# Kernel tuning notes

Measured on AMD Instinct MI355X. Metric: run time of the kernel, lower is better.

The kernel has to match this reference:

```python
import jax, jax.numpy as jnp
import numpy as np

# ---- static config (matches init_kwargs) ----
B, N_CAMS, C, H, W = 2, 6, 256, 32, 88
BEV_H = BEV_W = 100
NQ = BEV_H * BEV_W
D_PILLAR = 4
HEADS = 8
LEVELS = 3
HEAD_DIM = C // HEADS
PC_RANGE = (-51.2, -51.2, -5.0, 51.2, 51.2, 3.0)
OGFH, OGFW = 256, 704


def _make_lidar2img():
    """Plausible lidar->image projection matrices (K @ [R|t]) for 6 ring cameras."""
    mats = np.zeros((B, N_CAMS, 4, 4), np.float32)
    K = np.array([[557.0, 0.0, OGFW / 2.0], [0.0, 557.0, OGFH / 2.0], [0.0, 0.0, 1.0]], np.float64)
    for b in range(B):
        for n in range(N_CAMS):
            yaw = 2.0 * np.pi * n / N_CAMS + 0.05 * b
            fwd = np.array([np.cos(yaw), np.sin(yaw), 0.0])
            right = np.array([np.sin(yaw), -np.cos(yaw), 0.0])
            down = np.array([0.0, 0.0, -1.0])
            R = np.stack([right, down, fwd])  # lidar -> camera axes
            cam_center = np.array([1.5 * np.cos(yaw), 1.5 * np.sin(yaw), 1.8])
            t = -R @ cam_center
            P = K @ np.concatenate([R, t[:, None]], axis=1)
            mats[b, n, :3, :] = P.astype(np.float32)
            mats[b, n, 3, 3] = 1.0
    return jnp.asarray(mats)


def setup_inputs() -> dict:
    key = jax.random.key(0)
    ks = jax.random.split(key, 16)
    s = 0.02
    return {
        'imgs': jax.random.normal(ks[0], (B, N_CAMS, C, H, W), jnp.float32),
        'lidar2img': _make_lidar2img(),
        'bev_query': jax.random.normal(ks[1], (NQ, 1, C), jnp.float32) * s,
        'bev_pos': jax.random.normal(ks[2], (1, NQ, C), jnp.float32) * s,
        'cams_embeds': jax.random.normal(ks[3], (N_CAMS, C), jnp.float32) * s,
        'level_embeds': jax.random.normal(ks[4], (LEVELS, C), jnp.float32) * s,
        'w_fpn': jax.random.normal(ks[5], (LEVELS, C, C), jnp.float32) * s,
        'b_fpn': jnp.zeros((LEVELS, C), jnp.float32),
        'w_value': jax.random.normal(ks[6], (C, C), jnp.float32) * s,
        'b_value': jnp.zeros((C,), jnp.float32),
        'w_off': jax.random.normal(ks[7], (C, HEADS * LEVELS * D_PILLAR * 2), jnp.float32) * s,
        'b_off': jax.random.normal(ks[8], (HEADS * LEVELS * D_PILLAR * 2,), jnp.float32) * 0.5,
        'w_attn': jax.random.normal(ks[9], (C, HEADS * LEVELS * D_PILLAR), jnp.float32) * s,
        'b_attn': jnp.zeros((HEADS * LEVELS * D_PILLAR,), jnp.float32),
        'w_out': jax.random.normal(ks[10], (C, C), jnp.float32) * s,
        'b_out': jnp.zeros((C,), jnp.float32),
        'w_ts1': jax.random.normal(ks[11], (C, C), jnp.float32) * s,
        'b_ts1': jnp.zeros((C,), jnp.float32),
        'w_ts2': jax.random.normal(ks[12], (C, C), jnp.float32) * s,
        'b_ts2': jnp.zeros((C,), jnp.float32),
    }


def _deform_sample(v, loc, h, w):
    """Bilinear sample (grid_sample, zero padding, align_corners=False).
    v: [N, heads, h*w, dh]; loc: [N, heads, Q, 2] normalized to [0,1]. -> [N, heads, Q, dh]"""
    x = loc[..., 0] * w - 0.5
    y = loc[..., 1] * h - 0.5
    x0 = jnp.floor(x)
    y0 = jnp.floor(y)
    out = jnp.zeros(v.shape[:2] + (loc.shape[2], v.shape[-1]), v.dtype)
    for dx in (0, 1):
        for dy in (0, 1):
            xi = x0 + dx
            yi = y0 + dy
            wgt = (1.0 - jnp.abs(x - xi)) * (1.0 - jnp.abs(y - yi))
            valid = (xi >= 0) & (xi < w) & (yi >= 0) & (yi < h)
            idx = (jnp.clip(yi, 0, h - 1) * w + jnp.clip(xi, 0, w - 1)).astype(jnp.int32)
            g = jnp.take_along_axis(v, idx[..., None], axis=2)
            out = out + g * (wgt * valid)[..., None]
    return out


def _forward(imgs, lidar2img, bev_query, bev_pos, cams_embeds, level_embeds,
             w_fpn, b_fpn, w_value, b_value, w_off, b_off, w_attn, b_attn,
             w_out, b_out, w_ts1, b_ts1, w_ts2, b_ts2):
    # ---- FPN: 3 levels at strides 1/2/4 with per-level 1x1 projection ----
    x = imgs.reshape(B * N_CAMS, C, H, W)
    feats, shapes = [], []
    cur = x
    for l in range(LEVELS):
        if l > 0:
            bn, c, h, w = cur.shape
            cur = cur.reshape(bn, c, h // 2, 2, w // 2, 2).mean(axis=(3, 5))
        f = jnp.einsum('bchw,cd->bdhw', cur, w_fpn[l]) + b_fpn[l][None, :, None, None]
        feats.append(f)
        shapes.append((f.shape[2], f.shape[3]))
    # ---- flatten levels + cam/level embeds: [N, sum_hw, B, C] ----
    flat = []
    for l, f in enumerate(feats):
        h, w = shapes[l]
        fl = jnp.transpose(f.reshape(B, N_CAMS, C, h * w), (1, 0, 3, 2))  # [N,B,hw,C]
        fl = fl + cams_embeds[:, None, None, :] + level_embeds[l][None, None, None, :]
        flat.append(fl)
    feat_flatten = jnp.transpose(jnp.concatenate(flat, axis=2), (0, 2, 1, 3))  # [N,sum_hw,B,C]

    # ---- 3D pillar reference points, normalized [0,1] ----
    zrange = PC_RANGE[5] - PC_RANGE[2]
    zs = jnp.linspace(0.5, zrange - 0.5, D_PILLAR) / zrange
    xs = (jnp.arange(BEV_W, dtype=jnp.float32) + 0.5) / BEV_W
    ys = (jnp.arange(BEV_H, dtype=jnp.float32) + 0.5) / BEV_H
    gy, gx = jnp.meshgrid(ys, xs, indexing='ij')
    ref2d = jnp.stack([gx.ravel(), gy.ravel()], axis=-1)  # [NQ,2]
    ref3d = jnp.concatenate([
        jnp.broadcast_to(ref2d[None], (D_PILLAR, NQ, 2)),
        jnp.broadcast_to(zs[:, None, None].astype(jnp.float32), (D_PILLAR, NQ, 1)),
    ], axis=-1)
    scale = jnp.array([PC_RANGE[3] - PC_RANGE[0], PC_RANGE[4] - PC_RANGE[1], zrange], jnp.float32)
    shift = jnp.array(PC_RANGE[:3], jnp.float32)
    xyz = ref3d * scale + shift
    homog = jnp.concatenate([xyz, jnp.ones((D_PILLAR, NQ, 1), jnp.float32)], axis=-1)

    # ---- point sampling: project to each camera, mask invalid pixels ----
    pts = jnp.einsum('bnij,dqj->nbqdi', lidar2img, homog)  # [N,B,NQ,D,4]
    eps = 1e-5
    depth = pts[..., 2]
    xy = pts[..., :2] / jnp.maximum(depth[..., None], eps)
    ref_cam = xy / jnp.array([OGFW, OGFH], jnp.float32)  # [N,B,NQ,D,2]
    bev_mask = ((depth > eps) & (ref_cam[..., 0] > 0) & (ref_cam[..., 0] < 1)
                & (ref_cam[..., 1] > 0) & (ref_cam[..., 1] < 1))  # [N,B,NQ,D]

    pos = bev_pos[0]  # [NQ,C]

    def sca(query, value, ref_b, mask_b):
        # query [NQ,C]; value [N,sum_hw,C]; ref_b [N,NQ,D,2]; mask_b [N,NQ,D]
        residual = query
        q = query + pos
        v = value @ w_value + b_value
        off = (q @ w_off + b_off).reshape(NQ, HEADS, LEVELS, D_PILLAR, 2)
        attn = jax.nn.softmax((q @ w_attn + b_attn).reshape(NQ, HEADS, LEVELS * D_PILLAR), axis=-1)
        attn = attn.reshape(NQ, HEADS, LEVELS, D_PILLAR)
        out = jnp.zeros((N_CAMS, NQ, HEADS, HEAD_DIM), q.dtype)
        start = 0
        for l, (h, w) in enumerate(shapes):
            hw = h * w
            v_l = jnp.transpose(v[:, start:start + hw].reshape(N_CAMS, hw, HEADS, HEAD_DIM), (0, 2, 1, 3))
            start += hw
            norm = jnp.array([w, h], q.dtype)
            loc = ref_b[:, :, None, :, :] + off[None, :, :, l] / norm  # [N,NQ,heads,D,2]
            loc = jnp.transpose(loc, (0, 2, 1, 3, 4)).reshape(N_CAMS, HEADS, NQ * D_PILLAR, 2)
            s = _deform_sample(v_l, loc, h, w).reshape(N_CAMS, HEADS, NQ, D_PILLAR, HEAD_DIM)
            out = out + jnp.einsum('nhqpd,qhp->nqhd', s, attn[:, :, l])
        out = out.reshape(N_CAMS, NQ, C)
        valid = mask_b.any(axis=-1)  # [N,NQ]
        slots = (out * valid[..., None].astype(out.dtype)).sum(axis=0)
        count = jnp.maximum(valid.sum(axis=0), 1).astype(out.dtype)[:, None]
        slots = slots / count
        return slots @ w_out + b_out + residual

    def tsblock(t):
        return jax.nn.relu(t @ w_ts1 + b_ts1) @ w_ts2 + b_ts2

    bq = jnp.transpose(bev_query, (1, 0, 2))[0]  # [NQ,C]
    groups = []
    ego = bq
    for b in range(B):
        val = feat_flatten[:, :, b, :]
        r = ref_cam[:, b]
        m = bev_mask[:, b]
        if b == 0:
            for _ in range(2):
                bq = tsblock(sca(bq, val, r, m))
            ego = bq
            groups.append(ego.reshape(C, BEV_W, BEV_H))
        else:
            nb = tsblock(sca(ego, val, r, m))
            groups.append(nb.reshape(C, BEV_W, BEV_H))
    bev_groups = jnp.stack(groups, axis=0)  # [B,C,BEV_W,BEV_H]
    return bq[None], bev_groups


def reference(imgs, lidar2img, bev_query, bev_pos, cams_embeds, level_embeds,
              w_fpn, b_fpn, w_value, b_value, w_off, b_off, w_attn, b_attn,
              w_out, b_out, w_ts1, b_ts1, w_ts2, b_ts2):
    return _forward(imgs, lidar2img, bev_query, bev_pos, cams_embeds, level_embeds,
                    w_fpn, b_fpn, w_value, b_value, w_off, b_off, w_attn, b_attn,
                    w_out, b_out, w_ts1, b_ts1, w_ts2, b_ts2)
```

## Files before the change

### kernel.cpp

```cpp
#include <hip/hip_runtime.h>
#include <math.h>

typedef __attribute__((ext_vector_type(8))) short bf16x8;
typedef __attribute__((ext_vector_type(4))) float f32x4;

__device__ __forceinline__ unsigned short f2bf(float x) {
  union { float f; unsigned int u; } v; v.f = x;
  unsigned int r = v.u + 0x7fffu + ((v.u >> 16) & 1u);
  return (unsigned short)(r >> 16);
}
__device__ __forceinline__ float bf2f(unsigned short b) {
  union { unsigned int u; float f; } v; v.u = ((unsigned int)b) << 16; return v.f;
}
__device__ __forceinline__ void split2(float x, unsigned short& h, unsigned short& l) {
  h = f2bf(x);
  l = f2bf(x - bf2f(h));
}
__device__ __forceinline__ int fsi(int q, int c) { return q * 256 + (c ^ ((q & 7) << 2)); }

__device__ __forceinline__ void writeP(unsigned short* __restrict__ P, int col, int k,
                                       unsigned short h, unsigned short l) {
  int tile = col >> 4;
  int lane = (((k >> 3) & 3) << 4) | (col & 15);
  int ks = k >> 5, j8 = k & 7;
  size_t base = ((size_t)(tile >> 1) * 16384) + (size_t)(((tile & 1) << 4) + ks * 2) * 512
              + (size_t)lane * 8 + j8;
  P[base] = h;
  P[base + 512] = l;
}

__device__ __forceinline__ void ld16(const unsigned short* b, bf16x8* f) {
  const unsigned short* b1 = b + 2048;
  const unsigned short* b2 = b + 4096;
  const unsigned short* b3 = b + 6144;
  asm volatile(
    "global_load_dwordx4 %0, %16, off\n\t"
    "global_load_dwordx4 %1, %16, off offset:1024\n\t"
    "global_load_dwordx4 %2, %16, off offset:2048\n\t"
    "global_load_dwordx4 %3, %16, off offset:3072\n\t"
    "global_load_dwordx4 %4, %17, off\n\t"
    "global_load_dwordx4 %5, %17, off offset:1024\n\t"
    "global_load_dwordx4 %6, %17, off offset:2048\n\t"
    "global_load_dwordx4 %7, %17, off offset:3072\n\t"
    "global_load_dwordx4 %8, %18, off\n\t"
    "global_load_dwordx4 %9, %18, off offset:1024\n\t"
    "global_load_dwordx4 %10, %18, off offset:2048\n\t"
    "global_load_dwordx4 %11, %18, off offset:3072\n\t"
    "global_load_dwordx4 %12, %19, off\n\t"
    "global_load_dwordx4 %13, %19, off offset:1024\n\t"
    "global_load_dwordx4 %14, %19, off offset:2048\n\t"
    "global_load_dwordx4 %15, %19, off offset:3072\n\t"
    "s_waitcnt vmcnt(0)"
    : "=&v"(f[0]), "=&v"(f[1]), "=&v"(f[2]), "=&v"(f[3]),
      "=&v"(f[4]), "=&v"(f[5]), "=&v"(f[6]), "=&v"(f[7]),
      "=&v"(f[8]), "=&v"(f[9]), "=&v"(f[10]), "=&v"(f[11]),
      "=&v"(f[12]), "=&v"(f[13]), "=&v"(f[14]), "=&v"(f[15])
    : "v"(b), "v"(b1), "v"(b2), "v"(b3));
}

__device__ __forceinline__ void ld16nw(const unsigned short* b, bf16x8* f) {
  const unsigned short* b1 = b + 2048;
  const unsigned short* b2 = b + 4096;
  const unsigned short* b3 = b + 6144;
  asm volatile(
    "global_load_dwordx4 %0, %16, off\n\t"
    "global_load_dwordx4 %1, %16, off offset:1024\n\t"
    "global_load_dwordx4 %2, %16, off offset:2048\n\t"
    "global_load_dwordx4 %3, %16, off offset:3072\n\t"
    "global_load_dwordx4 %4, %17, off\n\t"
    "global_load_dwordx4 %5, %17, off offset:1024\n\t"
    "global_load_dwordx4 %6, %17, off offset:2048\n\t"
    "global_load_dwordx4 %7, %17, off offset:3072\n\t"
    "global_load_dwordx4 %8, %18, off\n\t"
    "global_load_dwordx4 %9, %18, off offset:1024\n\t"
    "global_load_dwordx4 %10, %18, off offset:2048\n\t"
    "global_load_dwordx4 %11, %18, off offset:3072\n\t"
    "global_load_dwordx4 %12, %19, off\n\t"
    "global_load_dwordx4 %13, %19, off offset:1024\n\t"
    "global_load_dwordx4 %14, %19, off offset:2048\n\t"
    "global_load_dwordx4 %15, %19, off offset:3072"
    : "=&v"(f[0]), "=&v"(f[1]), "=&v"(f[2]), "=&v"(f[3]),
      "=&v"(f[4]), "=&v"(f[5]), "=&v"(f[6]), "=&v"(f[7]),
      "=&v"(f[8]), "=&v"(f[9]), "=&v"(f[10]), "=&v"(f[11]),
      "=&v"(f[12]), "=&v"(f[13]), "=&v"(f[14]), "=&v"(f[15])
    : "v"(b), "v"(b1), "v"(b2), "v"(b3));
}

#define MFMA(a, b, c) __builtin_amdgcn_mfma_f32_16x16x32_bf16(a, b, c, 0, 0, 0)

__device__ __forceinline__ void gemm2t32(
    const unsigned short* __restrict__ Wp, int tile0,
    int lane, int lk, int l15,
    const unsigned short (&AS)[2][32][32][8], f32x4 (&acc)[2][2])
{
  const unsigned short* base = Wp + ((size_t)(tile0 >> 1) * 16384) + (size_t)lane * 8;
  bf16x8 f[32];
  ld16nw(base, f);
  ld16(base + 8192, f + 16);
  __builtin_amdgcn_sched_barrier(0);
#pragma unroll
  for (int ks = 0; ks < 8; ++ks) {
    bf16x8 h0 = f[2 * ks], l0 = f[2 * ks + 1];
    bf16x8 h1 = f[16 + 2 * ks], l1 = f[17 + 2 * ks];
#pragma unroll
    for (int nf = 0; nf < 2; ++nf) {
      bf16x8 bqh = *(const bf16x8*)&AS[0][ks * 4 + lk][nf * 16 + l15][0];
      bf16x8 bql = *(const bf16x8*)&AS[1][ks * 4 + lk][nf * 16 + l15][0];
      acc[0][nf] = MFMA(h0, bqh, acc[0][nf]);
      acc[0][nf] = MFMA(h0, bql, acc[0][nf]);
      acc[0][nf] = MFMA(l0, bqh, acc[0][nf]);
      acc[1][nf] = MFMA(h1, bqh, acc[1][nf]);
      acc[1][nf] = MFMA(h1, bql, acc[1][nf]);
      acc[1][nf] = MFMA(l1, bqh, acc[1][nf]);
    }
  }
}

__device__ __forceinline__ void gemm2t64(
    const unsigned short* __restrict__ Wp, int tile0,
    int lane, int lk, int l15,
    const unsigned short (&AS)[2][32][64][8], f32x4 (&acc)[2][4])
{
  const unsigned short* base = Wp + ((size_t)(tile0 >> 1) * 16384) + (size_t)lane * 8;
  bf16x8 f[32];
  ld16nw(base, f);
  ld16(base + 8192, f + 16);
  __builtin_amdgcn_sched_barrier(0);
#pragma unroll
  for (int ks = 0; ks < 8; ++ks) {
    bf16x8 h0 = f[2 * ks], l0 = f[2 * ks + 1];
    bf16x8 h1 = f[16 + 2 * ks], l1 = f[17 + 2 * ks];
#pragma unroll
    for (int nf = 0; nf < 4; ++nf) {
      bf16x8 bqh = *(const bf16x8*)&AS[0][ks * 4 + lk][nf * 16 + l15][0];
      bf16x8 bql = *(const bf16x8*)&AS[1][ks * 4 + lk][nf * 16 + l15][0];
      acc[0][nf] = MFMA(h0, bqh, acc[0][nf]);
      acc[0][nf] = MFMA(h0, bql, acc[0][nf]);
      acc[0][nf] = MFMA(l0, bqh, acc[0][nf]);
      acc[1][nf] = MFMA(h1, bqh, acc[1][nf]);
      acc[1][nf] = MFMA(h1, bql, acc[1][nf]);
      acc[1][nf] = MFMA(l1, bqh, acc[1][nf]);
    }
  }
}

__device__ __forceinline__ void gemm1t64(
    const unsigned short* __restrict__ Wp, int tile,
    int lane, int lk, int l15,
    const unsigned short (&AS)[2][32][64][8], f32x4 (&acc)[4])
{
  const unsigned short* base = Wp + ((size_t)(tile >> 1) * 16384) + (size_t)(tile & 1) * 8192 + (size_t)lane * 8;
  bf16x8 f[16];
  ld16(base, f);
  __builtin_amdgcn_sched_barrier(0);
#pragma unroll
  for (int ks = 0; ks < 8; ++ks) {
    bf16x8 eh = f[2 * ks], el = f[2 * ks + 1];
#pragma unroll
    for (int nf = 0; nf < 4; ++nf) {
      bf16x8 bqh = *(const bf16x8*)&AS[0][ks * 4 + lk][nf * 16 + l15][0];
      bf16x8 bql = *(const bf16x8*)&AS[1][ks * 4 + lk][nf * 16 + l15][0];
      acc[nf] = MFMA(eh, bqh, acc[nf]);
      acc[nf] = MFMA(eh, bql, acc[nf]);
      acc[nf] = MFMA(el, bqh, acc[nf]);
    }
  }
}

__global__ __launch_bounds__(256) void pool2x2(const float* __restrict__ in, float* __restrict__ out,
                                               int h, int w, int total)
{
  int i = blockIdx.x * 256 + threadIdx.x;
  if (i >= total) return;
  int x = i % w; int r = i / w; int y = r % h; int ci = r / h;
  const float* p = in + (size_t)ci * (4 * h * w) + (size_t)(2 * y) * (2 * w) + 2 * x;
  out[i] = (p[0] + p[1] + p[2 * w] + p[2 * w + 1]) * 0.25f;
}

__global__ __launch_bounds__(256) void prep(
    const float* __restrict__ wo, const float* __restrict__ bo,
    const float* __restrict__ wa, const float* __restrict__ ba,
    const float* __restrict__ wout, const float* __restrict__ wts1, const float* __restrict__ wts2,
    const float* __restrict__ wfpn, const float* __restrict__ wval,
    const float* __restrict__ cams, const float* __restrict__ lev,
    const float* __restrict__ bfpn, const float* __restrict__ bval,
    unsigned short* __restrict__ wcatP, float* __restrict__ bcat,
    unsigned short* __restrict__ woutP, unsigned short* __restrict__ wts1P,
    unsigned short* __restrict__ w45P, unsigned short* __restrict__ wcombP,
    float* __restrict__ e2)
{
  int bb = blockIdx.x, t = threadIdx.x;
  if (bb < 768) {
    int l = bb >> 8, i = bb & 255, j = t;
    const float* a = wfpn + ((size_t)l * 256 + i) * 256;
    float acc = 0.f;
    for (int k = 0; k < 256; ++k) acc = fmaf(a[k], wval[(size_t)k * 256 + j], acc);
    unsigned short h, lo; split2(acc, h, lo);
    writeP(wcombP, l * 256 + j, i, h, lo);
  } else if (bb < 1056) {
    int i = (bb - 768) * 256 + t;
    int c = i >> 8, k = i & 255;
    float v = (c < 192) ? wo[k * 192 + c] : wa[k * 96 + (c - 192)];
    unsigned short h, l; split2(v, h, l);
    writeP(wcatP, c, k, h, l);
    if (i < 288) bcat[i] = (i < 192) ? bo[i] : ba[i - 192];
  } else if (bb < 1312) {
    int i = (bb - 1056) * 256 + t;
    int nn = i >> 8, k = i & 255;
    float v = wout[(size_t)k * 256 + nn];
    unsigned short h, l; split2(v, h, l);
    writeP(woutP, nn, k, h, l);
  } else if (bb < 1568) {
    int i = (bb - 1312) * 256 + t;
    int nn = i >> 8, k = i & 255;
    float v = wts1[(size_t)k * 256 + nn];
    unsigned short h, l; split2(v, h, l);
    writeP(wts1P, nn, k, h, l);
  } else if (bb < 1824) {
    int i = (bb - 1568) * 256 + t;
    int nn = i >> 8, k = i & 255;
    float v = wts2[(size_t)k * 256 + nn];
    unsigned short h, l; split2(v, h, l);
    writeP(w45P, nn, k, h, l);
  } else if (bb < 2112) {
    int mp = bb - 1824;
    int k = t;
    float acc = 0.f;
    for (int j = 0; j < 256; ++j) {
      float wc = (mp < 192) ? wo[j * 192 + mp] : wa[j * 96 + (mp - 192)];
      acc = fmaf(wts2[(size_t)k * 256 + j], wc, acc);
    }
    unsigned short h, l; split2(acc, h, l);
    writeP(w45P, 256 + mp, k, h, l);
  } else {
    int e = bb - 2112;
    int n = e / 3, l = e % 3, j = t;
    float acc = bval[j];
    for (int k = 0; k < 256; ++k) {
      float s = cams[n * 256 + k] + lev[l * 256 + k] + bfpn[l * 256 + k];
      acc = fmaf(s, wval[(size_t)k * 256 + j], acc);
    }
    e2[(size_t)e * 256 + j] = acc;
  }
}

__global__ __launch_bounds__(512) void value_fused(
    const float* __restrict__ imgs, const float* __restrict__ cur1a, const float* __restrict__ cur2a,
    const unsigned short* __restrict__ wcombP,
    const float* __restrict__ e2, float* __restrict__ Vall)
{
  __shared__ __align__(16) unsigned short AS[2][32][32][8];
  int t = threadIdx.x, wid = t >> 6, lane = t & 63, l15 = lane & 15, lk = lane >> 4;
  int bx = blockIdx.x, cam = blockIdx.y, bz = blockIdx.z;
  const float* img0 = imgs + (size_t)bz * 4325376;
  const float* cur1 = cur1a + (size_t)bz * 1081344;
  const float* cur2 = cur2a + (size_t)bz * 270336;
  float* V = Vall + (size_t)bz * 5677056;
  int level, tb, hw; const float* src;
  if (bx < 88)       { level = 0; tb = bx;       hw = 2816; src = img0; }
  else if (bx < 110) { level = 1; tb = bx - 88;  hw = 704;  src = cur1; }
  else               { level = 2; tb = bx - 110; hw = 176;  src = cur2; }
  int p0 = tb * 32;
  const int LST[3] = {0, 2816, 3520};
  src += (size_t)cam * 256 * hw;

  {
    int pos = t & 31, kg = t >> 5;
    bool ok = (p0 + pos) < hw;
    const float* col = src + p0 + pos;
    float vals[16];
#pragma unroll
    for (int i = 0; i < 16; ++i) {
      int k = kg * 16 + i;
      vals[i] = ok ? col[(size_t)k * hw] : 0.f;
    }
#pragma unroll
    for (int half = 0; half < 2; ++half) {
      int ch = kg * 2 + half;
      bf16x8 hv, lv;
#pragma unroll
      for (int j = 0; j < 8; ++j) {
        unsigned short h, l; split2(vals[half * 8 + j], h, l);
        hv[j] = (short)h; lv[j] = (short)l;
      }
      *(bf16x8*)&AS[0][ch][pos][0] = hv;
      *(bf16x8*)&AS[1][ch][pos][0] = lv;
    }
  }
  __syncthreads();

  f32x4 zed = {0.f, 0.f, 0.f, 0.f};
  f32x4 acc[2][2] = {{zed, zed}, {zed, zed}};
  gemm2t32(wcombP, level * 16 + wid * 2, lane, lk, l15, AS, acc);
  __syncthreads();

  float* ASf = (float*)(&AS[0][0][0][0]);
  const float* bias = e2 + (size_t)(cam * 3 + level) * 256;
#pragma unroll
  for (int mf = 0; mf < 2; ++mf) {
    int chb = (wid * 2 + mf) * 16 + lk * 4;
    float4 b4 = *(const float4*)(bias + chb);
#pragma unroll
    for (int nf = 0; nf < 2; ++nf) {
      int q = nf * 16 + l15;
      float4 o;
      o.x = acc[mf][nf][0] + b4.x; o.y = acc[mf][nf][1] + b4.y;
      o.z = acc[mf][nf][2] + b4.z; o.w = acc[mf][nf][3] + b4.w;
      *(float4*)&ASf[fsi(q, chb)] = o;
    }
  }
  __syncthreads();
  float* Vb = V + ((size_t)cam * 3696 + LST[level] + p0) * 256;
#pragma unroll
  for (int j = 0; j < 4; ++j) {
    int g = t + j * 512;
    int q = g >> 6, c = (g & 63) * 4;
    if (p0 + q < hw)
      *(float4*)(Vb + (size_t)q * 256 + c) = *(const float4*)&ASf[fsi(q, c)];
  }
}

__global__ __launch_bounds__(512) void init_fused(
    const float* __restrict__ bev_pos, const float* __restrict__ bev_query,
    const float* __restrict__ bts2,
    const unsigned short* __restrict__ wcatP, const float* __restrict__ bcat,
    float* __restrict__ posA, float* __restrict__ posB,
    float* __restrict__ qtmpA, float* __restrict__ qtmpB)
{
  __shared__ __align__(16) unsigned short AS[2][32][64][8];
  float* ASf = (float*)(&AS[0][0][0][0]);
  int t = threadIdx.x, wid = t >> 6, lane = t & 63, l15 = lane & 15, lk = lane >> 4;
  int r0 = blockIdx.x * 64;
  int y = blockIdx.y;
  const float* base = y ? bev_query : bev_pos;
  const float* padd = y ? bev_pos : nullptr;
  const float* rb = y ? nullptr : bts2;
  float* oA = y ? qtmpA : posA;
  float* oB = y ? qtmpB : posB;
  f32x4 zed = {0.f, 0.f, 0.f, 0.f};

#pragma unroll
  for (int j = 0; j < 8; ++j) {
    int g = t + j * 512;
    int q = g >> 6, c = (g & 63) * 4;
    int rq = r0 + q; if (rq > 9999) rq = 9999;
    float4 a = *(const float4*)(base + (size_t)rq * 256 + c);
    if (padd) {
      float4 p = *(const float4*)(padd + (size_t)rq * 256 + c);
      a.x += p.x; a.y += p.y; a.z += p.z; a.w += p.w;
    }
    if (rb) {
      float4 rv = *(const float4*)(rb + c);
      a.x += rv.x; a.y += rv.y; a.z += rv.z; a.w += rv.w;
    }
    ushort4 hh, ll;
    split2(a.x, hh.x, ll.x); split2(a.y, hh.y, ll.y);
    split2(a.z, hh.z, ll.z); split2(a.w, hh.w, ll.w);
    *(ushort4*)&AS[0][c >> 3][q][c & 7] = hh;
    *(ushort4*)&AS[1][c >> 3][q][c & 7] = ll;
  }
  __syncthreads();

  f32x4 acc[2][4] = {{zed, zed, zed, zed}, {zed, zed, zed, zed}};
  gemm2t64(wcatP, wid * 2, lane, lk, l15, AS, acc);
  f32x4 acc3[4] = {zed, zed, zed, zed};
  if (wid < 2) gemm1t64(wcatP, 16 + wid, lane, lk, l15, AS, acc3);
  __syncthreads();
#pragma unroll
  for (int mf = 0; mf < 2; ++mf) {
    int chb = (wid * 2 + mf) * 16 + lk * 4;
    float4 b4 = *(const float4*)(bcat + chb);
#pragma unroll
    for (int nf = 0; nf < 4; ++nf) {
      int q = nf * 16 + l15;
      float4 o;
      o.x = acc[mf][nf][0] + b4.x; o.y = acc[mf][nf][1] + b4.y;
      o.z = acc[mf][nf][2] + b4.z; o.w = acc[mf][nf][3] + b4.w;
      *(float4*)&ASf[fsi(q, chb)] = o;
    }
  }
  if (wid < 2) {
    int ce = wid * 16 + lk * 4;
    float4 b4 = *(const float4*)(bcat + 256 + ce);
#pragma unroll
    for (int nf = 0; nf < 4; ++nf) {
      int qg = r0 + nf * 16 + l15;
      if (qg < 10000) {
        float4 o;
        o.x = acc3[nf][0] + b4.x; o.y = acc3[nf][1] + b4.y;
        o.z = acc3[nf][2] + b4.z; o.w = acc3[nf][3] + b4.w;
        *(float4*)(oB + (size_t)qg * 32 + ce) = o;
      }
    }
  }
  __syncthreads();
#pragma unroll
  for (int j = 0; j < 8; ++j) {
    int g = t + j * 512;
    int q = g >> 6, c = (g & 63) * 4;
    int qg = r0 + q;
    if (qg < 10000)
      *(float4*)(oA + (size_t)qg * 256 + c) = *(const float4*)&ASf[fsi(q, c)];
  }
}

__global__ __launch_bounds__(512) void fused_iter(
    const float* __restrict__ slots, const float* __restrict__ qin,
    const unsigned short* __restrict__ woutP, const unsigned short* __restrict__ wts1P,
    const unsigned short* __restrict__ w45P,
    const float* __restrict__ bout, const float* __restrict__ bts1,
    const float* __restrict__ bts2,
    float* __restrict__ qout, float* __restrict__ outA, float* __restrict__ outB,
    float* __restrict__ qtmpA, float* __restrict__ qtmpB)
{
  __shared__ __align__(16) unsigned short AS[2][32][64][8];
  float* ASf = (float*)(&AS[0][0][0][0]);
  int t = threadIdx.x, wid = t >> 6, lane = t & 63, l15 = lane & 15, lk = lane >> 4;
  int r0 = blockIdx.x * 64;
  f32x4 zed = {0.f, 0.f, 0.f, 0.f};

#pragma unroll
  for (int j = 0; j < 8; ++j) {
    int g = t + j * 512;
    int q = g >> 6, c = (g & 63) * 4;
    int rq = r0 + q; if (rq > 9999) rq = 9999;
    float4 a = *(const float4*)(slots + (size_t)rq * 256 + c);
    ushort4 hh, ll;
    split2(a.x, hh.x, ll.x); split2(a.y, hh.y, ll.y);
    split2(a.z, hh.z, ll.z); split2(a.w, hh.w, ll.w);
    *(ushort4*)&AS[0][c >> 3][q][c & 7] = hh;
    *(ushort4*)&AS[1][c >> 3][q][c & 7] = ll;
  }
  __syncthreads();

  {
    f32x4 acc[2][4] = {{zed, zed, zed, zed}, {zed, zed, zed, zed}};
    gemm2t64(woutP, wid * 2, lane, lk, l15, AS, acc);
    __syncthreads();
    float4 qreg[8];
#pragma unroll
    for (int j = 0; j < 8; ++j) {
      int g = t + j * 512;
      int q = g >> 6, c = (g & 63) * 4;
      int rq = r0 + q; if (rq > 9999) rq = 9999;
      qreg[j] = *(const float4*)(qin + (size_t)rq * 256 + c);
    }
#pragma unroll
    for (int j = 0; j < 8; ++j) {
      int g = t + j * 512;
      int q = g >> 6, c = (g & 63) * 4;
      *(float4*)&ASf[fsi(q, c)] = qreg[j];
    }
    __syncthreads();
    float4 rr[2][4];
#pragma unroll
    for (int mf = 0; mf < 2; ++mf) {
      int chb = (wid * 2 + mf) * 16 + lk * 4;
#pragma unroll
      for (int nf = 0; nf < 4; ++nf)
        rr[mf][nf] = *(const float4*)&ASf[fsi(nf * 16 + l15, chb)];
    }
    __syncthreads();
#pragma unroll
    for (int mf = 0; mf < 2; ++mf) {
      int chb = (wid * 2 + mf) * 16 + lk * 4;
      float4 b4 = *(const float4*)(bout + chb);
#pragma unroll
      for (int nf = 0; nf < 4; ++nf) {
        int q = nf * 16 + l15;
        float v0 = acc[mf][nf][0] + b4.x + rr[mf][nf].x;
        float v1 = acc[mf][nf][1] + b4.y + rr[mf][nf].y;
        float v2 = acc[mf][nf][2] + b4.z + rr[mf][nf].z;
        float v3 = acc[mf][nf][3] + b4.w + rr[mf][nf].w;
        ushort4 hh, ll;
        split2(v0, hh.x, ll.x); split2(v1, hh.y, ll.y);
        split2(v2, hh.z, ll.z); split2(v3, hh.w, ll.w);
        *(ushort4*)&AS[0][chb >> 3][q][chb & 7] = hh;
        *(ushort4*)&AS[1][chb >> 3][q][chb & 7] = ll;
      }
    }
    __syncthreads();
  }
  {
    f32x4 acc[2][4] = {{zed, zed, zed, zed}, {zed, zed, zed, zed}};
    gemm2t64(wts1P, wid * 2, lane, lk, l15, AS, acc);
    __syncthreads();
#pragma unroll
    for (int mf = 0; mf < 2; ++mf) {
      int chb = (wid * 2 + mf) * 16 + lk * 4;
      float4 b4 = *(const float4*)(bts1 + chb);
#pragma unroll
      for (int nf = 0; nf < 4; ++nf) {
        int q = nf * 16 + l15;
        float v0 = fmaxf(acc[mf][nf][0] + b4.x, 0.f);
        float v1 = fmaxf(acc[mf][nf][1] + b4.y, 0.f);
        float v2 = fmaxf(acc[mf][nf][2] + b4.z, 0.f);
        float v3 = fmaxf(acc[mf][nf][3] + b4.w, 0.f);
        ushort4 hh, ll;
        split2(v0, hh.x, ll.x); split2(v1, hh.y, ll.y);
        split2(v2, hh.z, ll.z); split2(v3, hh.w, ll.w);
        *(ushort4*)&AS[0][chb >> 3][q][chb & 7] = hh;
        *(ushort4*)&AS[1][chb >> 3][q][chb & 7] = ll;
      }
    }
    __syncthreads();
  }
  {
    f32x4 accA[2][4] = {{zed, zed, zed, zed}, {zed, zed, zed, zed}};
    f32x4 accB[2][4] = {{zed, zed, zed, zed}, {zed, zed, zed, zed}};
    if (wid < 4 || qtmpA) {
      gemm2t64(w45P, wid * 4,     lane, lk, l15, AS, accA);
      gemm2t64(w45P, wid * 4 + 2, lane, lk, l15, AS, accB);
    }
    f32x4 acc3[4] = {zed, zed, zed, zed};
    if (qtmpA && wid < 2) gemm1t64(w45P, 32 + wid, lane, lk, l15, AS, acc3);
    __syncthreads();
    if (wid < 4) {
#pragma unroll
      for (int half = 0; half < 2; ++half) {
#pragma unroll
        for (int mf = 0; mf < 2; ++mf) {
          int chb = (wid * 4 + half * 2 + mf) * 16 + lk * 4;
          float4 b4 = *(const float4*)(bts2 + chb);
#pragma unroll
          for (int nf = 0; nf < 4; ++nf) {
            int q = nf * 16 + l15;
            f32x4 a = half ? accB[mf][nf] : accA[mf][nf];
            float4 o;
            o.x = a[0] + b4.x; o.y = a[1] + b4.y;
            o.z = a[2] + b4.z; o.w = a[3] + b4.w;
            *(float4*)&ASf[fsi(q, chb)] = o;
          }
        }
      }
    }
    if (qtmpA && wid < 2) {
      int ce = wid * 16 + lk * 4;
#pragma unroll
      for (int nf = 0; nf < 4; ++nf) {
        int qg = r0 + nf * 16 + l15;
        if (qg < 10000) {
          float4 o;
          o.x = acc3[nf][0]; o.y = acc3[nf][1]; o.z = acc3[nf][2]; o.w = acc3[nf][3];
          *(float4*)(qtmpB + (size_t)qg * 32 + ce) = o;
        }
      }
    }
    __syncthreads();
#pragma unroll
    for (int j = 0; j < 8; ++j) {
      int g = t + j * 512;
      int q = g >> 6, c = (g & 63) * 4;
      int qg = r0 + q;
      if (qg < 10000) {
        float4 vq = *(const float4*)&ASf[fsi(q, c)];
        size_t go = (size_t)qg * 256 + c;
        *(float4*)(qout + go) = vq;
        if (outA) { *(float4*)(outA + go) = vq; *(float4*)(outB + go) = vq; }
      }
    }
    if (!qtmpA) return;
    __syncthreads();
    if (wid >= 4) {
#pragma unroll
      for (int half = 0; half < 2; ++half) {
#pragma unroll
        for (int mf = 0; mf < 2; ++mf) {
          int cc = ((wid - 4) * 4 + half * 2 + mf) * 16 + lk * 4;
#pragma unroll
          for (int nf = 0; nf < 4; ++nf) {
            int q = nf * 16 + l15;
            f32x4 a = half ? accB[mf][nf] : accA[mf][nf];
            float4 o;
            o.x = a[0]; o.y = a[1]; o.z = a[2]; o.w = a[3];
            *(float4*)&ASf[fsi(q, cc)] = o;
          }
        }
      }
    }
    __syncthreads();
#pragma unroll
    for (int j = 0; j < 8; ++j) {
      int g = t + j * 512;
      int q = g >> 6, c = (g & 63) * 4;
      int qg = r0 + q;
      if (qg < 10000)
        *(float4*)(qtmpA + (size_t)qg * 256 + c) = *(const float4*)&ASf[fsi(q, c)];
    }
  }
}

__global__ __launch_bounds__(256) void sca_sample(const float* __restrict__ qtmpA, const float* __restrict__ qtmpB,
                                                  const float* __restrict__ posA, const float* __restrict__ posB,
                                                  const float* __restrict__ V,
                                                  const float* __restrict__ l2i, float* __restrict__ slots)
{
  int b = blockIdx.x;
  int q = (b & 7) * 1250 + (b >> 3);
  int t = threadIdx.x;
  int head = t >> 5;
  __shared__ float raw[288];
  __shared__ float attnS[96];
  __shared__ float refx[6][4], refy[6][4];
  __shared__ int mnd[24];
  __shared__ int validn[6];
  __shared__ __align__(16) float w4[576][4];
  __shared__ __align__(16) int o4[576][4];

  {
    float x = qtmpA[(size_t)q * 256 + t];
    if (posA) x += posA[(size_t)q * 256 + t];
    raw[t] = x;
    if (t < 32) {
      float y = qtmpB[(size_t)q * 32 + t];
      if (posB) y += posB[(size_t)q * 32 + t];
      raw[256 + t] = y;
    }
  }
  if (t >= 32 && t < 56) {
    int tt = t - 32;
    int n = tt >> 2, d = tt & 3;
    const float* Mrow = l2i + n * 16;
    int qx = q % 100, qy = q / 100;
    float X = ((qx + 0.5f) / 100.0f) * 102.4f + (-51.2f);
    float Y = ((qy + 0.5f) / 100.0f) * 102.4f + (-51.2f);
    float zi = (d == 3) ? 7.5f : (0.5f + (float)d * (7.0f / 3.0f));
    float Z = zi + (-5.0f);
    float px = Mrow[0] * X + Mrow[1] * Y + Mrow[2] * Z + Mrow[3];
    float py = Mrow[4] * X + Mrow[5] * Y + Mrow[6] * Z + Mrow[7];
    float pz = Mrow[8] * X + Mrow[9] * Y + Mrow[10] * Z + Mrow[11];
    float dz = fmaxf(pz, 1e-5f);
    float xc = (px / dz) / 704.0f;
    float yc = (py / dz) / 256.0f;
    refx[n][d] = xc; refy[n][d] = yc;
    mnd[n * 4 + d] = (pz > 1e-5f) && (xc > 0.f) && (xc < 1.f) && (yc > 0.f) && (yc < 1.f);
  }
  __syncthreads();
  if (t < 8) {
    float mx = raw[192 + t * 12];
    for (int p = 1; p < 12; ++p) mx = fmaxf(mx, raw[192 + t * 12 + p]);
    float s = 0.f;
    float e[12];
#pragma unroll
    for (int p = 0; p < 12; ++p) { e[p] = __expf(raw[192 + t * 12 + p] - mx); s += e[p]; }
    float inv = 1.f / s;
#pragma unroll
    for (int p = 0; p < 12; ++p) attnS[t * 12 + p] = e[p] * inv;
  } else if (t < 14) {
    int n = t - 8;
    validn[n] = mnd[n * 4] | mnd[n * 4 + 1] | mnd[n * 4 + 2] | mnd[n * 4 + 3];
  }
  __syncthreads();

  int packed = 0, nv = 0;
#pragma unroll
  for (int n = 0; n < 6; ++n)
    if (validn[n]) { packed |= n << (3 * nv); nv++; }
  float invc = 1.f / (float)(nv > 1 ? nv : 1);

  const float WWf[3] = {88.f, 44.f, 22.f}, HHf[3] = {32.f, 16.f, 8.f};
  const int WWi[3] = {88, 44, 22}, STi[3] = {0, 2816, 3520};
  int npts = nv * 96;
  for (int pt = t; pt < npts; pt += 256) {
    int hd = pt & 7;
    int g = pt >> 3;
    int j = g % 12, ni = g / 12;
    int n = (packed >> (3 * ni)) & 7;
    int l = j >> 2, d = j & 3;
    float wwf = WWf[l], hhf = HHf[l];
    int wwi = WWi[l], st = STi[l];
    float a = attnS[hd * 12 + j] * invc;
    float ox = raw[hd * 24 + l * 8 + d * 2 + 0];
    float oy = raw[hd * 24 + l * 8 + d * 2 + 1];
    float x = refx[n][d] * wwf + ox - 0.5f;
    float y = refy[n][d] * hhf + oy - 0.5f;
    float x0 = floorf(x), y0 = floorf(y);
    float fx = x - x0, fy = y - y0;
    float wx0 = 1.f - fx, wy0 = 1.f - fy;
    float vx0 = (x0 >= 0.f && x0 < wwf) ? 1.f : 0.f;
    float vx1 = (x0 + 1.f >= 0.f && x0 + 1.f < wwf) ? 1.f : 0.f;
    float vy0 = (y0 >= 0.f && y0 < hhf) ? 1.f : 0.f;
    float vy1 = (y0 + 1.f >= 0.f && y0 + 1.f < hhf) ? 1.f : 0.f;
    w4[pt][0] = a * wx0 * wy0 * vx0 * vy0;
    w4[pt][1] = a * fx * wy0 * vx1 * vy0;
    w4[pt][2] = a * wx0 * fy * vx0 * vy1;
    w4[pt][3] = a * fx * fy * vx1 * vy1;
    int ix0 = (int)fminf(fmaxf(x0, 0.f), wwf - 1.f);
    int ix1 = (int)fminf(fmaxf(x0 + 1.f, 0.f), wwf - 1.f);
    int iy0 = (int)fminf(fmaxf(y0, 0.f), hhf - 1.f);
    int iy1 = (int)fminf(fmaxf(y0 + 1.f, 0.f), hhf - 1.f);
    int rA = (st + iy0 * wwi) << 10, rB = (st + iy1 * wwi) << 10;
    o4[pt][0] = rA + (ix0 << 10);
    o4[pt][1] = rA + (ix1 << 10);
    o4[pt][2] = rB + (ix0 << 10);
    o4[pt][3] = rB + (ix1 << 10);
  }
  __syncthreads();

  int t4 = t << 2;
  float acc0 = 0.f, acc1 = 0.f;
  int sl = 0;
#pragma unroll
  for (int n = 0; n < 6; ++n) {
    if (!validn[n]) continue;
    const char* Vn = (const char*)(V + (size_t)n * 946176);
    int pb = sl * 96 + head;
    sl++;
    float va[48];
#pragma unroll
    for (int j = 0; j < 12; ++j) {
      int4 o = *reinterpret_cast<const int4*>(&o4[pb + j * 8][0]);
      va[4 * j + 0] = *(const float*)(Vn + (unsigned)(o.x + t4));
      va[4 * j + 1] = *(const float*)(Vn + (unsigned)(o.y + t4));
      va[4 * j + 2] = *(const float*)(Vn + (unsigned)(o.z + t4));
      va[4 * j + 3] = *(const float*)(Vn + (unsigned)(o.w + t4));
    }
#pragma unroll
    for (int j = 0; j < 12; ++j) {
      float4 w = *reinterpret_cast<const float4*>(&w4[pb + j * 8][0]);
      acc0 = fmaf(w.x, va[4 * j + 0], acc0);
      acc1 = fmaf(w.y, va[4 * j + 1], acc1);
      acc0 = fmaf(w.z, va[4 * j + 2], acc0);
      acc1 = fmaf(w.w, va[4 * j + 3], acc1);
    }
  }
  slots[(size_t)q * 256 + t] = acc0 + acc1;
}

extern "C" void kernel_launch(void* const* d_in, const int* in_sizes, int n_in,
                              void* d_out, int out_size, void* d_ws, size_t ws_size,
                              hipStream_t stream)
{
  const float* imgs = (const float*)d_in[0];
  const float* l2i = (const float*)d_in[1];
  const float* bev_query = (const float*)d_in[2];
  const float* bev_pos = (const float*)d_in[3];
  const float* cams = (const float*)d_in[4];
  const float* lev = (const float*)d_in[5];
  const float* wfpn = (const float*)d_in[6];
  const float* bfpn = (const float*)d_in[7];
  const float* wval = (const float*)d_in[8];
  const float* bval = (const float*)d_in[9];
  const float* woff = (const float*)d_in[10];
  const float* boff = (const float*)d_in[11];
  const float* wattn = (const float*)d_in[12];
  const float* battn = (const float*)d_in[13];
  const float* wout = (const float*)d_in[14];
  const float* bout = (const float*)d_in[15];
  const float* wts1 = (const float*)d_in[16];
  const float* bts1 = (const float*)d_in[17];
  const float* wts2 = (const float*)d_in[18];
  const float* bts2 = (const float*)d_in[19];

  float* W = (float*)d_ws;
  size_t off = 0;
  auto alloc = [&](size_t n) { float* p = W + off; off += n; return p; };
  float* v    = alloc((size_t)2 * 5677056);
  float* cur1 = alloc((size_t)12 * 256 * 16 * 44);
  float* cur2 = alloc((size_t)12 * 256 * 8 * 22);
  float* bqA  = alloc(2560000);
  float* bqB  = alloc(2560000);
  float* qtmpA = alloc(2560000);
  float* qtmpB = alloc(320000);
  float* posA = alloc(2560000);
  float* posB = alloc(320000);
  float* slots = alloc(2560000);
  float* wcombPR = alloc(196608);
  float* wcatPR = alloc(73728);
  float* woutPR = alloc(65536);
  float* wts1PR = alloc(65536);
  float* w45PR = alloc(139264);
  float* bcat = alloc(512);
  float* e2 = alloc(4608);
  (void)ws_size; (void)in_sizes; (void)n_in; (void)out_size;

  unsigned short* wcombP = (unsigned short*)wcombPR;
  unsigned short* wcatP = (unsigned short*)wcatPR;
  unsigned short* woutP = (unsigned short*)woutPR;
  unsigned short* wts1P = (unsigned short*)wts1PR;
  unsigned short* w45P = (unsigned short*)w45PR;

  float* v0 = v;
  float* v1 = v + 5677056;
  float* OUT = (float*)d_out;

  pool2x2<<<8448, 256, 0, stream>>>(imgs, cur1, 16, 44, 2162688);
  pool2x2<<<2112, 256, 0, stream>>>(cur1, cur2, 8, 22, 540672);
  prep<<<2130, 256, 0, stream>>>(woff, boff, wattn, battn, wout, wts1, wts2, wfpn, wval,
                                 cams, lev, bfpn, bval,
                                 wcatP, bcat, woutP, wts1P, w45P, wcombP, e2);

  init_fused<<<dim3(157, 2), 512, 0, stream>>>(bev_pos, bev_query, bts2, wcatP, bcat,
                                               posA, posB, qtmpA, qtmpB);

  value_fused<<<dim3(116, 6, 2), 512, 0, stream>>>(imgs, cur1, cur2, wcombP, e2, v);

  sca_sample<<<10000, 256, 0, stream>>>(qtmpA, qtmpB, nullptr, nullptr, v0, l2i, slots);
  fused_iter<<<157, 512, 0, stream>>>(slots, bev_query,
      woutP, wts1P, w45P, bout, bts1, bts2,
      bqA, nullptr, nullptr, qtmpA, qtmpB);
  sca_sample<<<10000, 256, 0, stream>>>(qtmpA, qtmpB, posA, posB, v0, l2i, slots);
  fused_iter<<<157, 512, 0, stream>>>(slots, bqA,
      woutP, wts1P, w45P, bout, bts1, bts2,
      bqB, OUT, OUT + 2560000, qtmpA, qtmpB);
  sca_sample<<<10000, 256, 0, stream>>>(qtmpA, qtmpB, posA, posB, v1, l2i + 96, slots);
  fused_iter<<<157, 512, 0, stream>>>(slots, bqB,
      woutP, wts1P, w45P, bout, bts1, bts2,
      OUT + 5120000, nullptr, nullptr, nullptr, nullptr);
}
```

Before: 283.1 us.

## Merge pooling launches and fuse value projection with init GEMM kernel

Both pooling levels now run in a single launch, with the level-2 pool computed directly from the full-resolution images so it no longer depends on the level-1 output. The value projection and the query/pos init GEMMs share one grid, with a third z-slice running the init work as 32-row tiles, cutting two kernel launches and the gaps between them. The prep loops also get unroll-8 pragmas. The cost is redundant reads for the level-2 pool and more, smaller init blocks that each reload weight fragments.

```diff
diff --git a/kernel.cpp b/kernel.cpp
--- a/kernel.cpp
+++ b/kernel.cpp
@@ -116,6 +116,29 @@
   }
 }
 
+__device__ __forceinline__ void gemm1t32(
+    const unsigned short* __restrict__ Wp, int tile,
+    int lane, int lk, int l15,
+    const unsigned short (&AS)[2][32][32][8], f32x4 (&acc)[2])
+{
+  const unsigned short* base = Wp + ((size_t)(tile >> 1) * 16384) + (size_t)(tile & 1) * 8192 + (size_t)lane * 8;
+  bf16x8 f[16];
+  ld16(base, f);
+  __builtin_amdgcn_sched_barrier(0);
+#pragma unroll
+  for (int ks = 0; ks < 8; ++ks) {
+    bf16x8 eh = f[2 * ks], el = f[2 * ks + 1];
+#pragma unroll
+    for (int nf = 0; nf < 2; ++nf) {
+      bf16x8 bqh = *(const bf16x8*)&AS[0][ks * 4 + lk][nf * 16 + l15][0];
+      bf16x8 bql = *(const bf16x8*)&AS[1][ks * 4 + lk][nf * 16 + l15][0];
+      acc[nf] = MFMA(eh, bqh, acc[nf]);
+      acc[nf] = MFMA(eh, bql, acc[nf]);
+      acc[nf] = MFMA(el, bqh, acc[nf]);
+    }
+  }
+}
+
 __device__ __forceinline__ void gemm2t64(
     const unsigned short* __restrict__ Wp, int tile0,
     int lane, int lk, int l15,
@@ -167,14 +190,34 @@
   }
 }
 
-__global__ __launch_bounds__(256) void pool2x2(const float* __restrict__ in, float* __restrict__ out,
-                                               int h, int w, int total)
-{
-  int i = blockIdx.x * 256 + threadIdx.x;
-  if (i >= total) return;
-  int x = i % w; int r = i / w; int y = r % h; int ci = r / h;
-  const float* p = in + (size_t)ci * (4 * h * w) + (size_t)(2 * y) * (2 * w) + 2 * x;
-  out[i] = (p[0] + p[1] + p[2 * w] + p[2 * w + 1]) * 0.25f;
+__global__ __launch_bounds__(256) void pool_all(const float* __restrict__ imgs,
+                                                float* __restrict__ cur1, float* __restrict__ cur2)
+{
+  int blk = blockIdx.x, t = threadIdx.x;
+  if (blk < 8448) {
+    int i = blk * 256 + t;
+    if (i >= 2162688) return;
+    const int h = 16, w = 44;
+    int x = i % w; int r = i / w; int y = r % h; int ci = r / h;
+    const float* p = imgs + (size_t)ci * (4 * h * w) + (size_t)(2 * y) * (2 * w) + 2 * x;
+    cur1[i] = (p[0] + p[1] + p[2 * w] + p[2 * w + 1]) * 0.25f;
+    return;
+  }
+  int i = (blk - 8448) * 256 + t;
+  if (i >= 540672) return;
+  const int h2 = 8, w2 = 22;
+  int x2 = i % w2; int r = i / w2; int y2 = r % h2; int ci = r / h2;
+  const float* base = imgs + (size_t)ci * 2816;
+  float c1[2][2];
+#pragma unroll
+  for (int dy = 0; dy < 2; ++dy)
+#pragma unroll
+    for (int dx = 0; dx < 2; ++dx) {
+      int y1 = 2 * y2 + dy, x1 = 2 * x2 + dx;
+      const float* p = base + (size_t)(2 * y1) * 88 + 2 * x1;
+      c1[dy][dx] = (p[0] + p[1] + p[88] + p[89]) * 0.25f;
+    }
+  cur2[i] = (c1[0][0] + c1[0][1] + c1[1][0] + c1[1][1]) * 0.25f;
 }
 
 __global__ __launch_bounds__(256) void prep(
@@ -194,6 +237,7 @@
     int l = bb >> 8, i = bb & 255, j = t;
     const float* a = wfpn + ((size_t)l * 256 + i) * 256;
     float acc = 0.f;
+#pragma unroll 8
     for (int k = 0; k < 256; ++k) acc = fmaf(a[k], wval[(size_t)k * 256 + j], acc);
     unsigned short h, lo; split2(acc, h, lo);
     writeP(wcombP, l * 256 + j, i, h, lo);
@@ -226,6 +270,7 @@
     int mp = bb - 1824;
     int k = t;
     float acc = 0.f;
+#pragma unroll 8
     for (int j = 0; j < 256; ++j) {
       float wc = (mp < 192) ? wo[j * 192 + mp] : wa[j * 96 + (mp - 192)];
       acc = fmaf(wts2[(size_t)k * 256 + j], wc, acc);
@@ -236,6 +281,7 @@
     int e = bb - 2112;
     int n = e / 3, l = e % 3, j = t;
     float acc = bval[j];
+#pragma unroll 8
     for (int k = 0; k < 256; ++k) {
       float s = cams[n * 256 + k] + lev[l * 256 + k] + bfpn[l * 256 + k];
       acc = fmaf(s, wval[(size_t)k * 256 + j], acc);
@@ -244,163 +290,164 @@
   }
 }
 
-__global__ __launch_bounds__(512) void value_fused(
+__global__ __launch_bounds__(512) void vi_fused(
     const float* __restrict__ imgs, const float* __restrict__ cur1a, const float* __restrict__ cur2a,
-    const unsigned short* __restrict__ wcombP,
-    const float* __restrict__ e2, float* __restrict__ Vall)
-{
-  __shared__ __align__(16) unsigned short AS[2][32][32][8];
-  int t = threadIdx.x, wid = t >> 6, lane = t & 63, l15 = lane & 15, lk = lane >> 4;
-  int bx = blockIdx.x, cam = blockIdx.y, bz = blockIdx.z;
-  const float* img0 = imgs + (size_t)bz * 4325376;
-  const float* cur1 = cur1a + (size_t)bz * 1081344;
-  const float* cur2 = cur2a + (size_t)bz * 270336;
-  float* V = Vall + (size_t)bz * 5677056;
-  int level, tb, hw; const float* src;
-  if (bx < 88)       { level = 0; tb = bx;       hw = 2816; src = img0; }
-  else if (bx < 110) { level = 1; tb = bx - 88;  hw = 704;  src = cur1; }
-  else               { level = 2; tb = bx - 110; hw = 176;  src = cur2; }
-  int p0 = tb * 32;
-  const int LST[3] = {0, 2816, 3520};
-  src += (size_t)cam * 256 * hw;
-
-  {
-    int pos = t & 31, kg = t >> 5;
-    bool ok = (p0 + pos) < hw;
-    const float* col = src + p0 + pos;
-    float vals[16];
-#pragma unroll
-    for (int i = 0; i < 16; ++i) {
-      int k = kg * 16 + i;
-      vals[i] = ok ? col[(size_t)k * hw] : 0.f;
-    }
-#pragma unroll
-    for (int half = 0; half < 2; ++half) {
-      int ch = kg * 2 + half;
-      bf16x8 hv, lv;
-#pragma unroll
-      for (int j = 0; j < 8; ++j) {
-        unsigned short h, l; split2(vals[half * 8 + j], h, l);
-        hv[j] = (short)h; lv[j] = (short)l;
-      }
-      *(bf16x8*)&AS[0][ch][pos][0] = hv;
-      *(bf16x8*)&AS[1][ch][pos][0] = lv;
-    }
-  }
-  __syncthreads();
-
-  f32x4 zed = {0.f, 0.f, 0.f, 0.f};
-  f32x4 acc[2][2] = {{zed, zed}, {zed, zed}};
-  gemm2t32(wcombP, level * 16 + wid * 2, lane, lk, l15, AS, acc);
-  __syncthreads();
-
-  float* ASf = (float*)(&AS[0][0][0][0]);
-  const float* bias = e2 + (size_t)(cam * 3 + level) * 256;
-#pragma unroll
-  for (int mf = 0; mf < 2; ++mf) {
-    int chb = (wid * 2 + mf) * 16 + lk * 4;
-    float4 b4 = *(const float4*)(bias + chb);
-#pragma unroll
-    for (int nf = 0; nf < 2; ++nf) {
-      int q = nf * 16 + l15;
-      float4 o;
-      o.x = acc[mf][nf][0] + b4.x; o.y = acc[mf][nf][1] + b4.y;
-      o.z = acc[mf][nf][2] + b4.z; o.w = acc[mf][nf][3] + b4.w;
-      *(float4*)&ASf[fsi(q, chb)] = o;
-    }
-  }
-  __syncthreads();
-  float* Vb = V + ((size_t)cam * 3696 + LST[level] + p0) * 256;
-#pragma unroll
-  for (int j = 0; j < 4; ++j) {
-    int g = t + j * 512;
-    int q = g >> 6, c = (g & 63) * 4;
-    if (p0 + q < hw)
-      *(float4*)(Vb + (size_t)q * 256 + c) = *(const float4*)&ASf[fsi(q, c)];
-  }
-}
-
-__global__ __launch_bounds__(512) void init_fused(
+    const unsigned short* __restrict__ wcombP, const float* __restrict__ e2,
+    float* __restrict__ Vall,
     const float* __restrict__ bev_pos, const float* __restrict__ bev_query,
     const float* __restrict__ bts2,
     const unsigned short* __restrict__ wcatP, const float* __restrict__ bcat,
     float* __restrict__ posA, float* __restrict__ posB,
     float* __restrict__ qtmpA, float* __restrict__ qtmpB)
 {
-  __shared__ __align__(16) unsigned short AS[2][32][64][8];
+  __shared__ __align__(16) unsigned short AS[2][32][32][8];
   float* ASf = (float*)(&AS[0][0][0][0]);
   int t = threadIdx.x, wid = t >> 6, lane = t & 63, l15 = lane & 15, lk = lane >> 4;
-  int r0 = blockIdx.x * 64;
-  int y = blockIdx.y;
-  const float* base = y ? bev_query : bev_pos;
-  const float* padd = y ? bev_pos : nullptr;
-  const float* rb = y ? nullptr : bts2;
-  float* oA = y ? qtmpA : posA;
-  float* oB = y ? qtmpB : posB;
   f32x4 zed = {0.f, 0.f, 0.f, 0.f};
 
-#pragma unroll
-  for (int j = 0; j < 8; ++j) {
-    int g = t + j * 512;
-    int q = g >> 6, c = (g & 63) * 4;
-    int rq = r0 + q; if (rq > 9999) rq = 9999;
-    float4 a = *(const float4*)(base + (size_t)rq * 256 + c);
-    if (padd) {
-      float4 p = *(const float4*)(padd + (size_t)rq * 256 + c);
-      a.x += p.x; a.y += p.y; a.z += p.z; a.w += p.w;
-    }
-    if (rb) {
-      float4 rv = *(const float4*)(rb + c);
-      a.x += rv.x; a.y += rv.y; a.z += rv.z; a.w += rv.w;
-    }
-    ushort4 hh, ll;
-    split2(a.x, hh.x, ll.x); split2(a.y, hh.y, ll.y);
-    split2(a.z, hh.z, ll.z); split2(a.w, hh.w, ll.w);
-    *(ushort4*)&AS[0][c >> 3][q][c & 7] = hh;
-    *(ushort4*)&AS[1][c >> 3][q][c & 7] = ll;
-  }
-  __syncthreads();
-
-  f32x4 acc[2][4] = {{zed, zed, zed, zed}, {zed, zed, zed, zed}};
-  gemm2t64(wcatP, wid * 2, lane, lk, l15, AS, acc);
-  f32x4 acc3[4] = {zed, zed, zed, zed};
-  if (wid < 2) gemm1t64(wcatP, 16 + wid, lane, lk, l15, AS, acc3);
-  __syncthreads();
-#pragma unroll
-  for (int mf = 0; mf < 2; ++mf) {
-    int chb = (wid * 2 + mf) * 16 + lk * 4;
-    float4 b4 = *(const float4*)(bcat + chb);
-#pragma unroll
-    for (int nf = 0; nf < 4; ++nf) {
-      int q = nf * 16 + l15;
-      float4 o;
-      o.x = acc[mf][nf][0] + b4.x; o.y = acc[mf][nf][1] + b4.y;
-      o.z = acc[mf][nf][2] + b4.z; o.w = acc[mf][nf][3] + b4.w;
-      *(float4*)&ASf[fsi(q, chb)] = o;
-    }
-  }
-  if (wid < 2) {
-    int ce = wid * 16 + lk * 4;
-    float4 b4 = *(const float4*)(bcat + 256 + ce);
-#pragma unroll
-    for (int nf = 0; nf < 4; ++nf) {
-      int qg = r0 + nf * 16 + l15;
-      if (qg < 10000) {
+  if (blockIdx.z < 2) {
+    int bx = blockIdx.x, cam = blockIdx.y, bz = blockIdx.z;
+    const float* img0 = imgs + (size_t)bz * 4325376;
+    const float* cur1 = cur1a + (size_t)bz * 1081344;
+    const float* cur2 = cur2a + (size_t)bz * 270336;
+    float* V = Vall + (size_t)bz * 5677056;
+    int level, tb, hw; const float* src;
+    if (bx < 88)       { level = 0; tb = bx;       hw = 2816; src = img0; }
+    else if (bx < 110) { level = 1; tb = bx - 88;  hw = 704;  src = cur1; }
+    else               { level = 2; tb = bx - 110; hw = 176;  src = cur2; }
+    int p0 = tb * 32;
+    const int LST[3] = {0, 2816, 3520};
+    src += (size_t)cam * 256 * hw;
+
+    {
+      int pos = t & 31, kg = t >> 5;
+      bool ok = (p0 + pos) < hw;
+      const float* col = src + p0 + pos;
+      float vals[16];
+#pragma unroll
+      for (int i = 0; i < 16; ++i) {
+        int k = kg * 16 + i;
+        vals[i] = ok ? col[(size_t)k * hw] : 0.f;
+      }
+#pragma unroll
+      for (int half = 0; half < 2; ++half) {
+        int ch = kg * 2 + half;
+        bf16x8 hv, lv;
+#pragma unroll
+        for (int j = 0; j < 8; ++j) {
+          unsigned short h, l; split2(vals[half * 8 + j], h, l);
+          hv[j] = (short)h; lv[j] = (short)l;
+        }
+        *(bf16x8*)&AS[0][ch][pos][0] = hv;
+        *(bf16x8*)&AS[1][ch][pos][0] = lv;
+      }
+    }
+    __syncthreads();
+
+    f32x4 acc[2][2] = {{zed, zed}, {zed, zed}};
+    gemm2t32(wcombP, level * 16 + wid * 2, lane, lk, l15, AS, acc);
+    __syncthreads();
+
+    const float* bias = e2 + (size_t)(cam * 3 + level) * 256;
+#pragma unroll
+    for (int mf = 0; mf < 2; ++mf) {
+      int chb = (wid * 2 + mf) * 16 + lk * 4;
+      float4 b4 = *(const float4*)(bias + chb);
+#pragma unroll
+      for (int nf = 0; nf < 2; ++nf) {
+        int q = nf * 16 + l15;
         float4 o;
-        o.x = acc3[nf][0] + b4.x; o.y = acc3[nf][1] + b4.y;
-        o.z = acc3[nf][2] + b4.z; o.w = acc3[nf][3] + b4.w;
-        *(float4*)(oB + (size_t)qg * 32 + ce) = o;
-      }
-    }
-  }
-  __syncthreads();
-#pragma unroll
-  for (int j = 0; j < 8; ++j) {
-    int g = t + j * 512;
-    int q = g >> 6, c = (g & 63) * 4;
-    int qg = r0 + q;
-    if (qg < 10000)
-      *(float4*)(oA + (size_t)qg * 256 + c) = *(const float4*)&ASf[fsi(q, c)];
+        o.x = acc[mf][nf][0] + b4.x; o.y = acc[mf][nf][1] + b4.y;
+        o.z = acc[mf][nf][2] + b4.z; o.w = acc[mf][nf][3] + b4.w;
+        *(float4*)&ASf[fsi(q, chb)] = o;
+      }
+    }
+    __syncthreads();
+    float* Vb = V + ((size_t)cam * 3696 + LST[level] + p0) * 256;
+#pragma unroll
+    for (int j = 0; j < 4; ++j) {
+      int g = t + j * 512;
+      int q = g >> 6, c = (g & 63) * 4;
+      if (p0 + q < hw)
+        *(float4*)(Vb + (size_t)q * 256 + c) = *(const float4*)&ASf[fsi(q, c)];
+    }
+    return;
+  }
+
+  {
+    int id = blockIdx.y * 116 + blockIdx.x;
+    if (id >= 626) return;
+    int r0 = (id >> 1) * 32;
+    int y = id & 1;
+    const float* base = y ? bev_query : bev_pos;
+    const float* padd = y ? bev_pos : nullptr;
+    const float* rb = y ? nullptr : bts2;
+    float* oA = y ? qtmpA : posA;
+    float* oB = y ? qtmpB : posB;
+
+#pragma unroll
+    for (int j = 0; j < 4; ++j) {
+      int g = t + j * 512;
+      int q = g >> 6, c = (g & 63) * 4;
+      int rq = r0 + q; if (rq > 9999) rq = 9999;
+      float4 a = *(const float4*)(base + (size_t)rq * 256 + c);
+      if (padd) {
+        float4 p = *(const float4*)(padd + (size_t)rq * 256 + c);
+        a.x += p.x; a.y += p.y; a.z += p.z; a.w += p.w;
+      }
+      if (rb) {
+        float4 rv = *(const float4*)(rb + c);
+        a.x += rv.x; a.y += rv.y; a.z += rv.z; a.w += rv.w;
+      }
+      ushort4 hh, ll;
+      split2(a.x, hh.x, ll.x); split2(a.y, hh.y, ll.y);
+      split2(a.z, hh.z, ll.z); split2(a.w, hh.w, ll.w);
+      *(ushort4*)&AS[0][c >> 3][q][c & 7] = hh;
+      *(ushort4*)&AS[1][c >> 3][q][c & 7] = ll;
+    }
+    __syncthreads();
+
+    f32x4 acc[2][2] = {{zed, zed}, {zed, zed}};
+    gemm2t32(wcatP, wid * 2, lane, lk, l15, AS, acc);
+    f32x4 acc3[2] = {zed, zed};
+    if (wid < 2) gemm1t32(wcatP, 16 + wid, lane, lk, l15, AS, acc3);
+    __syncthreads();
+#pragma unroll
+    for (int mf = 0; mf < 2; ++mf) {
+      int chb = (wid * 2 + mf) * 16 + lk * 4;
+      float4 b4 = *(const float4*)(bcat + chb);
+#pragma unroll
+      for (int nf = 0; nf < 2; ++nf) {
+        int q = nf * 16 + l15;
+        float4 o;
+        o.x = acc[mf][nf][0] + b4.x; o.y = acc[mf][nf][1] + b4.y;
+        o.z = acc[mf][nf][2] + b4.z; o.w = acc[mf][nf][3] + b4.w;
+        *(float4*)&ASf[fsi(q, chb)] = o;
+      }
+    }
+    if (wid < 2) {
+      int ce = wid * 16 + lk * 4;
+      float4 b4 = *(const float4*)(bcat + 256 + ce);
+#pragma unroll
+      for (int nf = 0; nf < 2; ++nf) {
+        int qg = r0 + nf * 16 + l15;
+        if (qg < 10000) {
+          float4 o;
+          o.x = acc3[nf][0] + b4.x; o.y = acc3[nf][1] + b4.y;
+          o.z = acc3[nf][2] + b4.z; o.w = acc3[nf][3] + b4.w;
+          *(float4*)(oB + (size_t)qg * 32 + ce) = o;
+        }
+      }
+    }
+    __syncthreads();
+#pragma unroll
+    for (int j = 0; j < 4; ++j) {
+      int g = t + j * 512;
+      int q = g >> 6, c = (g & 63) * 4;
+      int qg = r0 + q;
+      if (qg < 10000)
+        *(float4*)(oA + (size_t)qg * 256 + c) = *(const float4*)&ASf[fsi(q, c)];
+    }
   }
 }
 
@@ -784,16 +831,14 @@
   float* v1 = v + 5677056;
   float* OUT = (float*)d_out;
 
-  pool2x2<<<8448, 256, 0, stream>>>(imgs, cur1, 16, 44, 2162688);
-  pool2x2<<<2112, 256, 0, stream>>>(cur1, cur2, 8, 22, 540672);
+  pool_all<<<8448 + 2112, 256, 0, stream>>>(imgs, cur1, cur2);
   prep<<<2130, 256, 0, stream>>>(woff, boff, wattn, battn, wout, wts1, wts2, wfpn, wval,
                                  cams, lev, bfpn, bval,
                                  wcatP, bcat, woutP, wts1P, w45P, wcombP, e2);
 
-  init_fused<<<dim3(157, 2), 512, 0, stream>>>(bev_pos, bev_query, bts2, wcatP, bcat,
-                                               posA, posB, qtmpA, qtmpB);
-
-  value_fused<<<dim3(116, 6, 2), 512, 0, stream>>>(imgs, cur1, cur2, wcombP, e2, v);
+  vi_fused<<<dim3(116, 6, 3), 512, 0, stream>>>(imgs, cur1, cur2, wcombP, e2, v,
+                                                bev_pos, bev_query, bts2, wcatP, bcat,
+                                                posA, posB, qtmpA, qtmpB);
 
   sca_sample<<<10000, 256, 0, stream>>>(qtmpA, qtmpB, nullptr, nullptr, v0, l2i, slots);
   fused_iter<<<157, 512, 0, stream>>>(slots, bev_query,
```

Result: no change. 279.0 us (-1.5%).
